# Kernel tuning notes

Hardware: AMD Instinct MI355X
Metric: run time of the kernel (lower is better)

## Reference

```python
import jax, jax.numpy as jnp
import numpy as np

N = 100000
E = 1600000
EPS = 1e-5

def setup_inputs() -> dict:
    key = jax.random.key(0)
    ks = jax.random.split(key, 10)
    d_in, d_h, d_out = 128, 128, 64
    sc = lambda d: 1.0 / np.sqrt(d)
    return {
        "x": jax.random.normal(ks[0], (N, d_in), jnp.float32),
        "edge_src": jax.random.randint(ks[1], (E,), 0, N, jnp.int32),
        "edge_dst": jax.random.randint(ks[2], (E,), 0, N, jnp.int32),
        "Wr0": jax.random.normal(ks[3], (d_in, d_h), jnp.float32) * sc(d_in),
        "Wn0": jax.random.normal(ks[4], (d_in, d_h), jnp.float32) * sc(d_in),
        "b0": jnp.zeros((d_h,), jnp.float32),
        "g0": jnp.ones((d_h,), jnp.float32),
        "be0": jnp.zeros((d_h,), jnp.float32),
        "Wr1": jax.random.normal(ks[5], (d_h, d_h), jnp.float32) * sc(d_h),
        "Wn1": jax.random.normal(ks[6], (d_h, d_h), jnp.float32) * sc(d_h),
        "b1": jnp.zeros((d_h,), jnp.float32),
        "g1": jnp.ones((d_h,), jnp.float32),
        "be1": jnp.zeros((d_h,), jnp.float32),
        "Wr2": jax.random.normal(ks[7], (d_h, d_out), jnp.float32) * sc(d_h),
        "Wn2": jax.random.normal(ks[8], (d_h, d_out), jnp.float32) * sc(d_h),
        "b2": jnp.zeros((d_out,), jnp.float32),
    }

def _mean_agg(x, src, dst):
    # GraphSAGE mean aggregation: scatter-mean of source features onto dst nodes
    deg = jax.ops.segment_sum(jnp.ones((src.shape[0],), x.dtype), dst, num_segments=N)
    s = jax.ops.segment_sum(x[src], dst, num_segments=N)  # [N, d] gather+scatter
    return s / jnp.maximum(deg, 1.0)[:, None]

def _sage_conv(x, src, dst, Wr, Wn, b):
    return x @ Wr + _mean_agg(x, src, dst) @ Wn + b

def _layernorm(h, g, b):
    mu = h.mean(-1, keepdims=True)
    var = ((h - mu) ** 2).mean(-1, keepdims=True)
    return (h - mu) * jax.lax.rsqrt(var + EPS) * g + b

def reference(x, edge_src, edge_dst, Wr0, Wn0, b0, g0, be0,
              Wr1, Wn1, b1, g1, be1, Wr2, Wn2, b2):
    # layer 0: conv -> dropout(eval=identity) -> LayerNorm -> relu
    h = _sage_conv(x, edge_src, edge_dst, Wr0, Wn0, b0)
    h = jax.nn.relu(_layernorm(h, g0, be0))
    # layer 1
    h = _sage_conv(h, edge_src, edge_dst, Wr1, Wn1, b1)
    h = jax.nn.relu(_layernorm(h, g1, be1))
    # final conv + log_softmax over classes
    h = _sage_conv(h, edge_src, edge_dst, Wr2, Wn2, b2)
    return jax.nn.log_softmax(h, axis=1)
```

## Files before the change

### kernel.cpp

```cpp
#include <hip/hip_runtime.h>
#include <math.h>

#define N_NODES 100000
#define NPAD 100032
#define N_EDGES 1600000
#define EPS 1e-5f
#define NC 256
#define CHUNK 6250
#define NR 98
#define RSZ 1024
#define NRC (NR * NC)
#define EIXL_CAP 1792

typedef __bf16 bf16x8 __attribute__((ext_vector_type(8)));
typedef float f32x4 __attribute__((ext_vector_type(4)));
typedef float f32x2 __attribute__((ext_vector_type(2)));

__device__ inline unsigned short f2bf(float f) {
    unsigned u = __float_as_uint(f);
    unsigned r = u + 0x7fffu + ((u >> 16) & 1u);
    return (unsigned short)(r >> 16);
}
__device__ inline float bflo(unsigned u) { return __uint_as_float(u << 16); }
__device__ inline float bfhi(unsigned u) { return __uint_as_float(u & 0xffff0000u); }
__device__ inline unsigned pack2(float lo, float hi) {
    return (unsigned)f2bf(lo) | ((unsigned)f2bf(hi) << 16);
}
__device__ inline unsigned char f2fp8(float f) {
    return (unsigned char)(__builtin_amdgcn_cvt_pk_fp8_f32(f, f, 0, false) & 0xff);
}

__global__ __launch_bounds__(256) void k_prep(const float* __restrict__ x,
                                              unsigned short* __restrict__ xb,
                                              unsigned* __restrict__ xq8,
                                              const int* __restrict__ dst,
                                              int* __restrict__ cntG) {
    __shared__ int hist[NR];
    int t = threadIdx.x;
    if (blockIdx.x < 12500) {
        int idx = blockIdx.x * 256 + t;
        float4 v = ((const float4*)x)[idx];
        ushort4 o;
        o.x = f2bf(v.x); o.y = f2bf(v.y); o.z = f2bf(v.z); o.w = f2bf(v.w);
        ((ushort4*)xb)[idx] = o;
        int q = __builtin_amdgcn_cvt_pk_fp8_f32(v.x, v.y, 0, false);
        q = __builtin_amdgcn_cvt_pk_fp8_f32(v.z, v.w, q, true);
        xq8[idx] = (unsigned)q;
    } else {
        int c = blockIdx.x - 12500;
        for (int i = t; i < NR; i += 256) hist[i] = 0;
        __syncthreads();
        int base = c * CHUNK;
        for (int i = base + t; i < base + CHUNK; i += 256)
            atomicAdd(&hist[dst[i] >> 10], 1);
        __syncthreads();
        for (int i = t; i < NR; i += 256) cntG[i * NC + c] = hist[i];
    }
}

__global__ __launch_bounds__(256) void k_scanA_prepw(
        int* __restrict__ cntG,
        const float* __restrict__ Wr0, const float* __restrict__ Wn0,
        const float* __restrict__ Wr1, const float* __restrict__ Wn1,
        const float* __restrict__ Wr2, const float* __restrict__ Wn2,
        unsigned short* __restrict__ WT0, unsigned short* __restrict__ WT1,
        unsigned short* __restrict__ WT2) {
    int t = threadIdx.x;
    if (blockIdx.x == 0) {
        __shared__ int ts[256];
        const int PER = NRC / 256;
        int s = 0;
        for (int i = 0; i < PER; ++i) s += cntG[t * PER + i];
        ts[t] = s;
        __syncthreads();
        #pragma unroll
        for (int off = 1; off < 256; off <<= 1) {
            int y = 0;
            if (t >= off) y = ts[t - off];
            __syncthreads();
            if (t >= off) ts[t] += y;
            __syncthreads();
        }
        int run = ts[t] - s;
        for (int i = 0; i < PER; ++i) {
            int v = cntG[t * PER + i];
            cntG[t * PER + i] = run;
            run += v;
        }
    } else {
        int b = blockIdx.x - 1;
        if (b < 256) {
            const float* Wr = (b < 128) ? Wr0 : Wr1;
            const float* Wn = (b < 128) ? Wn0 : Wn1;
            unsigned short* WT = (b < 128) ? WT0 : WT1;
            int idx = (b & 127) * 256 + t;
            int n = idx >> 8;
            int kc = idx & 255;
            float v = (kc < 128) ? Wr[kc * 128 + n] : Wn[(kc - 128) * 128 + n];
            WT[idx] = f2bf(v);
        } else {
            int idx = (b - 256) * 256 + t;
            int n = idx >> 7;
            int k = idx & 127;
            float v = (n < 64) ? Wr2[k * 64 + n] : Wn2[k * 64 + (n - 64)];
            WT2[n * 128 + k] = f2bf(v);
        }
    }
}

__global__ __launch_bounds__(1024) void k_bin(const int* __restrict__ src,
                                              const int* __restrict__ dst,
                                              const int* __restrict__ baseG,
                                              unsigned* __restrict__ bpack) {
    __shared__ int cur[NR];
    int t = threadIdx.x, c = blockIdx.x;
    for (int i = t; i < NR; i += 1024) cur[i] = baseG[i * NC + c];
    __syncthreads();
    int base = c * CHUNK;
    for (int i = base + t; i < base + CHUNK; i += 1024) {
        int d = dst[i];
        unsigned s = (unsigned)src[i];
        int p = atomicAdd(&cur[d >> 10], 1);
        bpack[p] = (s << 10) | (unsigned)(d & 1023);
    }
}

__global__ __launch_bounds__(1024) void k_nodeplace(
        const unsigned* __restrict__ bpack, const int* __restrict__ baseG,
        int* __restrict__ deg, float* __restrict__ invdeg,
        int* __restrict__ rowptr, int* __restrict__ eidx) {
    __shared__ int hist[RSZ];
    __shared__ int cur[RSZ];
    __shared__ int wbase[16];
    int r = blockIdx.x, t = threadIdx.x;
    hist[t] = 0;
    __syncthreads();
    int s0 = baseG[r * NC];
    int s1 = (r == NR - 1) ? N_EDGES : baseG[(r + 1) * NC];
    int nbase = r << 10;
    for (int i = s0 + t; i < s1; i += 1024)
        atomicAdd(&hist[bpack[i] & 1023u], 1);
    __syncthreads();
    int lane = t & 63, wv = t >> 6;
    int d = hist[t];
    int s = d;
    #pragma unroll
    for (int m = 1; m < 64; m <<= 1) {
        int y = __shfl_up(s, m);
        if (lane >= m) s += y;
    }
    if (lane == 63) wbase[wv] = s;
    __syncthreads();
    if (t < 16) {
        int v = wbase[t];
        int sv = v;
        #pragma unroll
        for (int m = 1; m < 16; m <<= 1) {
            int y = __shfl_up(sv, m);
            if (t >= m) sv += y;
        }
        wbase[t] = sv - v;
    }
    __syncthreads();
    int p = s0 + wbase[wv] + s - d;
    cur[t] = p;
    int n = nbase + t;
    if (n < N_NODES) {
        rowptr[n] = p;
        deg[n] = d;
        invdeg[n] = 1.0f / fmaxf((float)d, 1.0f);
    }
    __syncthreads();
    for (int i = s0 + t; i < s1; i += 1024) {
        unsigned bp = bpack[i];
        int pp = atomicAdd(&cur[bp & 1023u], 1);
        eidx[pp] = (int)(bp >> 10);
    }
}

__global__ __launch_bounds__(512, 8) void k_gemm_ln(
        const unsigned short* __restrict__ hb,
        const uint4* __restrict__ hq4,
        const int* __restrict__ eidx, const int* __restrict__ rowptr,
        const int* __restrict__ deg, const float* __restrict__ invdeg,
        const unsigned short* __restrict__ WT,
        const float* __restrict__ b, const float* __restrict__ g,
        const float* __restrict__ be, unsigned short* __restrict__ outb,
        unsigned char* __restrict__ outq8) {
    __shared__ unsigned short al[64][136];
    __shared__ unsigned short bt[128][40];
    __shared__ float p1[2][64], p2[2][64];
    __shared__ int eixl[EIXL_CAP];

    const int tid = threadIdx.x;
    const int lane = tid & 63;
    const int w = tid >> 6;
    const int quad = lane >> 4;
    const int l15 = lane & 15;
    const int rt = w >> 1;
    const int ch = w & 1;
    const int row0 = blockIdx.x * 64;

    bf16x8 selfA[4];
    {
        const unsigned short* base = hb + (size_t)(row0 + rt * 16 + l15) * 128 + quad * 8;
        #pragma unroll
        for (int kt = 0; kt < 4; ++kt)
            selfA[kt] = *(const bf16x8*)(base + kt * 32);
    }

    int e0 = rowptr[row0];
    int e1 = (row0 + 64 < N_NODES) ? rowptr[row0 + 64] : N_EDGES;
    int nE = e1 - e0;
    int staged = nE < EIXL_CAP ? nE : EIXL_CAP;
    for (int i = tid; i < staged; i += 512) eixl[i] = eidx[e0 + i];
    __syncthreads();

    {
        int r = tid >> 3;
        int l = tid & 7;
        int node = row0 + r;
        uint4 o0 = {0, 0, 0, 0}, o1 = {0, 0, 0, 0};
        if (node < N_NODES) {
            int start = rowptr[node];
            int cnt = deg[node];
            int rel = start - e0;
            f32x2 a[8];
            #pragma unroll
            for (int i = 0; i < 8; ++i) a[i] = (f32x2)0.0f;
            auto accum = [&](uint4 u) {
                a[0] += __builtin_amdgcn_cvt_pk_f32_fp8((int)u.x, false);
                a[1] += __builtin_amdgcn_cvt_pk_f32_fp8((int)u.x, true);
                a[2] += __builtin_amdgcn_cvt_pk_f32_fp8((int)u.y, false);
                a[3] += __builtin_amdgcn_cvt_pk_f32_fp8((int)u.y, true);
                a[4] += __builtin_amdgcn_cvt_pk_f32_fp8((int)u.z, false);
                a[5] += __builtin_amdgcn_cvt_pk_f32_fp8((int)u.z, true);
                a[6] += __builtin_amdgcn_cvt_pk_f32_fp8((int)u.w, false);
                a[7] += __builtin_amdgcn_cvt_pk_f32_fp8((int)u.w, true);
            };
            if (rel + cnt <= staged) {
                int j = 0;
                for (; j + 4 <= cnt; j += 4) {
                    int i0 = eixl[rel + j + 0], i1 = eixl[rel + j + 1];
                    int i2 = eixl[rel + j + 2], i3 = eixl[rel + j + 3];
                    uint4 u0 = hq4[(unsigned)(i0 * 8 + l)];
                    uint4 u1 = hq4[(unsigned)(i1 * 8 + l)];
                    uint4 u2 = hq4[(unsigned)(i2 * 8 + l)];
                    uint4 u3 = hq4[(unsigned)(i3 * 8 + l)];
                    accum(u0); accum(u1); accum(u2); accum(u3);
                }
                for (; j < cnt; ++j) {
                    uint4 u = hq4[(unsigned)(eixl[rel + j] * 8 + l)];
                    accum(u);
                }
            } else {
                int j = 0;
                for (; j + 4 <= cnt; j += 4) {
                    int s0 = eidx[start + j];
                    int s1 = eidx[start + j + 1];
                    int s2 = eidx[start + j + 2];
                    int s3 = eidx[start + j + 3];
                    uint4 u0 = hq4[(unsigned)(s0 * 8 + l)];
                    uint4 u1 = hq4[(unsigned)(s1 * 8 + l)];
                    uint4 u2 = hq4[(unsigned)(s2 * 8 + l)];
                    uint4 u3 = hq4[(unsigned)(s3 * 8 + l)];
                    accum(u0); accum(u1); accum(u2); accum(u3);
                }
                for (; j < cnt; ++j) {
                    uint4 u = hq4[(unsigned)(eidx[start + j] * 8 + l)];
                    accum(u);
                }
            }
            float id = invdeg[node];
            o0.x = pack2(a[0].x * id, a[0].y * id);
            o0.y = pack2(a[1].x * id, a[1].y * id);
            o0.z = pack2(a[2].x * id, a[2].y * id);
            o0.w = pack2(a[3].x * id, a[3].y * id);
            o1.x = pack2(a[4].x * id, a[4].y * id);
            o1.y = pack2(a[5].x * id, a[5].y * id);
            o1.z = pack2(a[6].x * id, a[6].y * id);
            o1.w = pack2(a[7].x * id, a[7].y * id);
        }
        *(uint4*)&al[r][l * 16] = o0;
        *(uint4*)&al[r][l * 16 + 8] = o1;
    }

    f32x4 acc[4];
    #pragma unroll
    for (int t = 0; t < 4; ++t)
        #pragma unroll
        for (int r = 0; r < 4; ++r) acc[t][r] = 0.0f;

    #pragma unroll
    for (int kt = 0; kt < 8; ++kt) {
        __syncthreads();
        {
            int n = tid >> 2;
            int c = tid & 3;
            *(float4*)&bt[n][c * 8] = ((const float4*)WT)[n * 32 + kt * 4 + c];
        }
        __syncthreads();
        bf16x8 a = (kt < 4)
            ? selfA[kt]
            : *(const bf16x8*)&al[rt * 16 + l15][(kt - 4) * 32 + quad * 8];
        #pragma unroll
        for (int t = 0; t < 4; ++t) {
            bf16x8 bb = *(const bf16x8*)&bt[ch * 64 + t * 16 + l15][quad * 8];
            acc[t] = __builtin_amdgcn_mfma_f32_16x16x32_bf16(a, bb, acc[t], 0, 0, 0);
        }
    }

    float bcol[4], gc[4], bec[4];
    #pragma unroll
    for (int t = 0; t < 4; ++t) {
        int col = ch * 64 + t * 16 + l15;
        bcol[t] = b[col]; gc[t] = g[col]; bec[t] = be[col];
    }
    float v[4][4];
    float s1[4], s2[4];
    #pragma unroll
    for (int r = 0; r < 4; ++r) { s1[r] = 0.0f; s2[r] = 0.0f; }
    #pragma unroll
    for (int t = 0; t < 4; ++t)
        #pragma unroll
        for (int r = 0; r < 4; ++r) {
            float x = acc[t][r] + bcol[t];
            v[t][r] = x;
            s1[r] += x;
            s2[r] += x * x;
        }
    #pragma unroll
    for (int m = 1; m <= 8; m <<= 1)
        #pragma unroll
        for (int r = 0; r < 4; ++r) {
            s1[r] += __shfl_xor(s1[r], m);
            s2[r] += __shfl_xor(s2[r], m);
        }
    if (l15 == 0) {
        #pragma unroll
        for (int r = 0; r < 4; ++r) {
            int rl = rt * 16 + quad * 4 + r;
            p1[ch][rl] = s1[r];
            p2[ch][rl] = s2[r];
        }
    }
    __syncthreads();
    #pragma unroll
    for (int r = 0; r < 4; ++r) {
        int rl = rt * 16 + quad * 4 + r;
        float S1 = p1[0][rl] + p1[1][rl];
        float S2 = p2[0][rl] + p2[1][rl];
        float mean = S1 * (1.0f / 128.0f);
        float var = S2 * (1.0f / 128.0f) - mean * mean;
        float rstd = rsqrtf(var + EPS);
        #pragma unroll
        for (int t = 0; t < 4; ++t) {
            int col = ch * 64 + t * 16 + l15;
            float o = fmaxf((v[t][r] - mean) * rstd * gc[t] + bec[t], 0.0f);
            outb[(size_t)(row0 + rl) * 128 + col] = f2bf(o);
            if (outq8) outq8[(size_t)(row0 + rl) * 128 + col] = f2fp8(o);
        }
    }
}

__global__ __launch_bounds__(512) void k_gemm2(
        const unsigned short* __restrict__ hb, const unsigned short* __restrict__ WT,
        const float* __restrict__ b2, unsigned short* __restrict__ zb16,
        unsigned char* __restrict__ yq8) {
    __shared__ unsigned short hl[64][136];
    __shared__ unsigned short bt[128][136];

    const int tid = threadIdx.x;
    const int lane = tid & 63;
    const int w = tid >> 6;
    const int quad = lane >> 4;
    const int l15 = lane & 15;
    const int rt = w >> 1;
    const int ch = w & 1;
    const int row0 = blockIdx.x * 64;

    #pragma unroll
    for (int t = 0; t < 2; ++t) {
        int idx = tid + t * 512;
        int r = idx >> 4;
        int c8 = idx & 15;
        *(float4*)&hl[r][c8 * 8] = ((const float4*)hb)[(size_t)(row0 + r) * 16 + c8];
    }
    #pragma unroll
    for (int t = 0; t < 4; ++t) {
        int idx = tid + t * 512;
        int n = idx >> 4;
        int c8 = idx & 15;
        *(float4*)&bt[n][c8 * 8] = ((const float4*)WT)[n * 16 + c8];
    }
    __syncthreads();

    f32x4 acc[4];
    #pragma unroll
    for (int t = 0; t < 4; ++t)
        #pragma unroll
        for (int r = 0; r < 4; ++r) acc[t][r] = 0.0f;

    #pragma unroll
    for (int ks = 0; ks < 4; ++ks) {
        bf16x8 a = *(const bf16x8*)&hl[rt * 16 + l15][ks * 32 + quad * 8];
        #pragma unroll
        for (int t = 0; t < 4; ++t) {
            bf16x8 bb = *(const bf16x8*)&bt[ch * 64 + t * 16 + l15][ks * 32 + quad * 8];
            acc[t] = __builtin_amdgcn_mfma_f32_16x16x32_bf16(a, bb, acc[t], 0, 0, 0);
        }
    }

    if (ch == 0) {
        #pragma unroll
        for (int t = 0; t < 4; ++t) {
            int col = t * 16 + l15;
            float bc = b2[col];
            #pragma unroll
            for (int r = 0; r < 4; ++r) {
                int rl = rt * 16 + quad * 4 + r;
                zb16[(size_t)(row0 + rl) * 64 + col] = f2bf(acc[t][r] + bc);
            }
        }
    } else {
        #pragma unroll
        for (int t = 0; t < 4; ++t) {
            int col = t * 16 + l15;
            #pragma unroll
            for (int r = 0; r < 4; ++r) {
                int rl = rt * 16 + quad * 4 + r;
                yq8[(size_t)(row0 + rl) * 64 + col] = f2fp8(acc[t][r]);
            }
        }
    }
}

__global__ __launch_bounds__(256) void k_l2g(const uint4* __restrict__ yq4,
                                             const unsigned short* __restrict__ zb16,
                                             const int* __restrict__ eidx,
                                             const int* __restrict__ rowptr,
                                             const int* __restrict__ deg,
                                             const float* __restrict__ invdeg,
                                             float* __restrict__ out) {
    __shared__ int eixl[EIXL_CAP];
    int node0 = blockIdx.x * 64;
    int e0 = rowptr[node0];
    int e1 = (node0 + 64 < N_NODES) ? rowptr[node0 + 64] : N_EDGES;
    int nE = e1 - e0;
    int staged = nE < EIXL_CAP ? nE : EIXL_CAP;
    for (int i = threadIdx.x; i < staged; i += 256) eixl[i] = eidx[e0 + i];
    __syncthreads();

    int node = node0 + (threadIdx.x >> 2);
    if (node >= N_NODES) return;
    int l = threadIdx.x & 3;
    int start = rowptr[node];
    int cnt = deg[node];
    int rel = start - e0;
    f32x2 a[8];
    #pragma unroll
    for (int i = 0; i < 8; ++i) a[i] = (f32x2)0.0f;

    auto accum = [&](uint4 u) {
        a[0] += __builtin_amdgcn_cvt_pk_f32_fp8((int)u.x, false);
        a[1] += __builtin_amdgcn_cvt_pk_f32_fp8((int)u.x, true);
        a[2] += __builtin_amdgcn_cvt_pk_f32_fp8((int)u.y, false);
        a[3] += __builtin_amdgcn_cvt_pk_f32_fp8((int)u.y, true);
        a[4] += __builtin_amdgcn_cvt_pk_f32_fp8((int)u.z, false);
        a[5] += __builtin_amdgcn_cvt_pk_f32_fp8((int)u.z, true);
        a[6] += __builtin_amdgcn_cvt_pk_f32_fp8((int)u.w, false);
        a[7] += __builtin_amdgcn_cvt_pk_f32_fp8((int)u.w, true);
    };

    if (rel + cnt <= staged) {
        int nb = cnt >> 3;
        for (int bq = 0; bq < nb; ++bq) {
            int jb = rel + bq * 8;
            int i0 = eixl[jb + 0], i1 = eixl[jb + 1];
            int i2 = eixl[jb + 2], i3 = eixl[jb + 3];
            int i4 = eixl[jb + 4], i5 = eixl[jb + 5];
            int i6 = eixl[jb + 6], i7 = eixl[jb + 7];
            uint4 u0 = yq4[(unsigned)(i0 * 4 + l)];
            uint4 u1 = yq4[(unsigned)(i1 * 4 + l)];
            uint4 u2 = yq4[(unsigned)(i2 * 4 + l)];
            uint4 u3 = yq4[(unsigned)(i3 * 4 + l)];
            uint4 u4 = yq4[(unsigned)(i4 * 4 + l)];
            uint4 u5 = yq4[(unsigned)(i5 * 4 + l)];
            uint4 u6 = yq4[(unsigned)(i6 * 4 + l)];
            uint4 u7 = yq4[(unsigned)(i7 * 4 + l)];
            accum(u0); accum(u1); accum(u2); accum(u3);
            accum(u4); accum(u5); accum(u6); accum(u7);
        }
        int j = nb << 3;
        int rem = cnt - j;
        #pragma unroll
        for (int k = 0; k < 8; ++k) {
            if (k < rem) {
                uint4 u = yq4[(unsigned)(eixl[rel + j + k] * 4 + l)];
                accum(u);
            }
        }
    } else {
        int j = 0;
        for (; j + 4 <= cnt; j += 4) {
            int s0 = eidx[start + j];
            int s1 = eidx[start + j + 1];
            int s2 = eidx[start + j + 2];
            int s3 = eidx[start + j + 3];
            uint4 u0 = yq4[(unsigned)(s0 * 4 + l)];
            uint4 u1 = yq4[(unsigned)(s1 * 4 + l)];
            uint4 u2 = yq4[(unsigned)(s2 * 4 + l)];
            uint4 u3 = yq4[(unsigned)(s3 * 4 + l)];
            accum(u0); accum(u1); accum(u2); accum(u3);
        }
        for (; j < cnt; ++j) {
            uint4 u = yq4[(unsigned)(eidx[start + j] * 4 + l)];
            accum(u);
        }
    }

    float id = invdeg[node];
    uint4 z0 = ((const uint4*)zb16)[(size_t)node * 8 + l * 2];
    uint4 z1 = ((const uint4*)zb16)[(size_t)node * 8 + l * 2 + 1];
    float v[16];
    v[0]  = bflo(z0.x) + a[0].x * id; v[1]  = bfhi(z0.x) + a[0].y * id;
    v[2]  = bflo(z0.y) + a[1].x * id; v[3]  = bfhi(z0.y) + a[1].y * id;
    v[4]  = bflo(z0.z) + a[2].x * id; v[5]  = bfhi(z0.z) + a[2].y * id;
    v[6]  = bflo(z0.w) + a[3].x * id; v[7]  = bfhi(z0.w) + a[3].y * id;
    v[8]  = bflo(z1.x) + a[4].x * id; v[9]  = bfhi(z1.x) + a[4].y * id;
    v[10] = bflo(z1.y) + a[5].x * id; v[11] = bfhi(z1.y) + a[5].y * id;
    v[12] = bflo(z1.z) + a[6].x * id; v[13] = bfhi(z1.z) + a[6].y * id;
    v[14] = bflo(z1.w) + a[7].x * id; v[15] = bfhi(z1.w) + a[7].y * id;

    float m = v[0];
    #pragma unroll
    for (int i = 1; i < 16; ++i) m = fmaxf(m, v[i]);
    m = fmaxf(m, __shfl_xor(m, 1));
    m = fmaxf(m, __shfl_xor(m, 2));
    float s = 0.0f;
    #pragma unroll
    for (int i = 0; i < 16; ++i) s += __expf(v[i] - m);
    s += __shfl_xor(s, 1);
    s += __shfl_xor(s, 2);
    float L = m + logf(s);
    #pragma unroll
    for (int k = 0; k < 4; ++k) {
        float4 o;
        o.x = v[4 * k] - L; o.y = v[4 * k + 1] - L;
        o.z = v[4 * k + 2] - L; o.w = v[4 * k + 3] - L;
        ((float4*)out)[(size_t)node * 16 + l * 4 + k] = o;
    }
}

extern "C" void kernel_launch(void* const* d_in, const int* in_sizes, int n_in,
                              void* d_out, int out_size, void* d_ws, size_t ws_size,
                              hipStream_t stream) {
    const float* x   = (const float*)d_in[0];
    const int* esrc  = (const int*)d_in[1];
    const int* edst  = (const int*)d_in[2];
    const float* Wr0 = (const float*)d_in[3];
    const float* Wn0 = (const float*)d_in[4];
    const float* b0  = (const float*)d_in[5];
    const float* g0  = (const float*)d_in[6];
    const float* be0 = (const float*)d_in[7];
    const float* Wr1 = (const float*)d_in[8];
    const float* Wn1 = (const float*)d_in[9];
    const float* b1  = (const float*)d_in[10];
    const float* g1  = (const float*)d_in[11];
    const float* be1 = (const float*)d_in[12];
    const float* Wr2 = (const float*)d_in[13];
    const float* Wn2 = (const float*)d_in[14];
    const float* b2  = (const float*)d_in[15];
    float* out = (float*)d_out;

    char* p = (char*)d_ws;
    auto alloc = [&](size_t bytes) {
        void* r = (void*)p;
        p += (bytes + 255) & ~(size_t)255;
        return r;
    };
    int*   deg    = (int*)  alloc(N_NODES * 4);
    float* invdeg = (float*)alloc(N_NODES * 4);
    int*   rowptr = (int*)  alloc(N_NODES * 4);
    int*   cntG   = (int*)  alloc(NRC * 4);
    unsigned* bpack = (unsigned*)alloc((size_t)N_EDGES * 4);
    int*   eidx   = (int*)  alloc((size_t)N_EDGES * 4);
    unsigned short* xb   = (unsigned short*)alloc((size_t)NPAD * 128 * 2);
    unsigned short* h1   = (unsigned short*)alloc((size_t)NPAD * 128 * 2);
    unsigned*       xq8  = (unsigned*)      alloc((size_t)N_NODES * 128);
    unsigned char*  h1q8 = (unsigned char*) alloc((size_t)NPAD * 128);
    unsigned short* zb16 = (unsigned short*)alloc((size_t)NPAD * 64 * 2);
    unsigned char*  yq8  = (unsigned char*) alloc((size_t)NPAD * 64);
    unsigned short* WT0  = (unsigned short*)alloc(128 * 256 * 2);
    unsigned short* WT1  = (unsigned short*)alloc(128 * 256 * 2);
    unsigned short* WT2  = (unsigned short*)alloc(128 * 128 * 2);

    k_prep<<<12500 + NC, 256, 0, stream>>>(x, xb, xq8, edst, cntG);
    k_scanA_prepw<<<321, 256, 0, stream>>>(cntG, Wr0, Wn0, Wr1, Wn1, Wr2, Wn2,
                                           WT0, WT1, WT2);
    k_bin<<<NC, 1024, 0, stream>>>(esrc, edst, cntG, bpack);
    k_nodeplace<<<NR, 1024, 0, stream>>>(bpack, cntG, deg, invdeg, rowptr, eidx);

    k_gemm_ln<<<NPAD / 64, 512, 0, stream>>>(xb, (const uint4*)xq8, eidx, rowptr,
                                             deg, invdeg, WT0, b0, g0, be0, h1, h1q8);

    k_gemm_ln<<<NPAD / 64, 512, 0, stream>>>(h1, (const uint4*)h1q8, eidx, rowptr,
                                             deg, invdeg, WT1, b1, g1, be1, xb,
                                             (unsigned char*)nullptr);

    k_gemm2<<<NPAD / 64, 512, 0, stream>>>(xb, WT2, b2, zb16, yq8);
    k_l2g<<<(N_NODES + 63) / 64, 256, 0, stream>>>((const uint4*)yq8, zb16, eidx, rowptr, deg, invdeg, out);
}
```

Before: 320.1 us.

## Fuse final layer GEMM into second gemm_ln kernel epilogue

The layer-2 GEMM (projecting the normalized hidden state into the self and neighbor 64-wide outputs) is folded into the second k_gemm_ln call. The LayerNorm+ReLU output is written to shared memory instead of global bf16, then multiplied against WT2 read directly from global memory. This removes one kernel launch and a full write and re-read of the 100k x 128 bf16 hidden tensor. In exchange, launch bounds drop from 8 to 6 waves per SIMD to leave room for extra registers, and B-operand loads now hit global/cache rather than LDS.

```diff
diff --git a/kernel.cpp b/kernel.cpp
--- a/kernel.cpp
+++ b/kernel.cpp
@@ -178,7 +178,7 @@
     }
 }
 
-__global__ __launch_bounds__(512, 8) void k_gemm_ln(
+__global__ __launch_bounds__(512, 6) void k_gemm_ln(
         const unsigned short* __restrict__ hb,
         const uint4* __restrict__ hq4,
         const int* __restrict__ eidx, const int* __restrict__ rowptr,
@@ -186,7 +186,11 @@
         const unsigned short* __restrict__ WT,
         const float* __restrict__ b, const float* __restrict__ g,
         const float* __restrict__ be, unsigned short* __restrict__ outb,
-        unsigned char* __restrict__ outq8) {
+        unsigned char* __restrict__ outq8,
+        const unsigned short* __restrict__ WT2,
+        const float* __restrict__ b2,
+        unsigned short* __restrict__ zb16,
+        unsigned char* __restrict__ yq8) {
     __shared__ unsigned short al[64][136];
     __shared__ unsigned short bt[128][40];
     __shared__ float p1[2][64], p2[2][64];
@@ -357,79 +361,52 @@
         for (int t = 0; t < 4; ++t) {
             int col = ch * 64 + t * 16 + l15;
             float o = fmaxf((v[t][r] - mean) * rstd * gc[t] + bec[t], 0.0f);
-            outb[(size_t)(row0 + rl) * 128 + col] = f2bf(o);
-            if (outq8) outq8[(size_t)(row0 + rl) * 128 + col] = f2fp8(o);
-        }
-    }
-}
-
-__global__ __launch_bounds__(512) void k_gemm2(
-        const unsigned short* __restrict__ hb, const unsigned short* __restrict__ WT,
-        const float* __restrict__ b2, unsigned short* __restrict__ zb16,
-        unsigned char* __restrict__ yq8) {
-    __shared__ unsigned short hl[64][136];
-    __shared__ unsigned short bt[128][136];
-
-    const int tid = threadIdx.x;
-    const int lane = tid & 63;
-    const int w = tid >> 6;
-    const int quad = lane >> 4;
-    const int l15 = lane & 15;
-    const int rt = w >> 1;
-    const int ch = w & 1;
-    const int row0 = blockIdx.x * 64;
-
-    #pragma unroll
-    for (int t = 0; t < 2; ++t) {
-        int idx = tid + t * 512;
-        int r = idx >> 4;
-        int c8 = idx & 15;
-        *(float4*)&hl[r][c8 * 8] = ((const float4*)hb)[(size_t)(row0 + r) * 16 + c8];
-    }
-    #pragma unroll
-    for (int t = 0; t < 4; ++t) {
-        int idx = tid + t * 512;
-        int n = idx >> 4;
-        int c8 = idx & 15;
-        *(float4*)&bt[n][c8 * 8] = ((const float4*)WT)[n * 16 + c8];
-    }
-    __syncthreads();
-
-    f32x4 acc[4];
-    #pragma unroll
-    for (int t = 0; t < 4; ++t)
-        #pragma unroll
-        for (int r = 0; r < 4; ++r) acc[t][r] = 0.0f;
-
-    #pragma unroll
-    for (int ks = 0; ks < 4; ++ks) {
-        bf16x8 a = *(const bf16x8*)&hl[rt * 16 + l15][ks * 32 + quad * 8];
-        #pragma unroll
-        for (int t = 0; t < 4; ++t) {
-            bf16x8 bb = *(const bf16x8*)&bt[ch * 64 + t * 16 + l15][ks * 32 + quad * 8];
-            acc[t] = __builtin_amdgcn_mfma_f32_16x16x32_bf16(a, bb, acc[t], 0, 0, 0);
-        }
-    }
-
-    if (ch == 0) {
-        #pragma unroll
-        for (int t = 0; t < 4; ++t) {
-            int col = t * 16 + l15;
-            float bc = b2[col];
+            if (!WT2) {
+                outb[(size_t)(row0 + rl) * 128 + col] = f2bf(o);
+                if (outq8) outq8[(size_t)(row0 + rl) * 128 + col] = f2fp8(o);
+            } else {
+                al[rl][col] = f2bf(o);
+            }
+        }
+    }
+
+    if (WT2) {
+        __syncthreads();
+        f32x4 acc2[4];
+        #pragma unroll
+        for (int t = 0; t < 4; ++t)
             #pragma unroll
-            for (int r = 0; r < 4; ++r) {
-                int rl = rt * 16 + quad * 4 + r;
-                zb16[(size_t)(row0 + rl) * 64 + col] = f2bf(acc[t][r] + bc);
+            for (int r = 0; r < 4; ++r) acc2[t][r] = 0.0f;
+        #pragma unroll
+        for (int kt = 0; kt < 4; ++kt) {
+            bf16x8 a = *(const bf16x8*)&al[rt * 16 + l15][kt * 32 + quad * 8];
+            #pragma unroll
+            for (int t = 0; t < 4; ++t) {
+                bf16x8 bb = *(const bf16x8*)(WT2 +
+                    (size_t)(ch * 64 + t * 16 + l15) * 128 + kt * 32 + quad * 8);
+                acc2[t] = __builtin_amdgcn_mfma_f32_16x16x32_bf16(a, bb, acc2[t], 0, 0, 0);
             }
         }
-    } else {
-        #pragma unroll
-        for (int t = 0; t < 4; ++t) {
-            int col = t * 16 + l15;
+        if (ch == 0) {
             #pragma unroll
-            for (int r = 0; r < 4; ++r) {
-                int rl = rt * 16 + quad * 4 + r;
-                yq8[(size_t)(row0 + rl) * 64 + col] = f2fp8(acc[t][r]);
+            for (int t = 0; t < 4; ++t) {
+                int col = t * 16 + l15;
+                float bc = b2[col];
+                #pragma unroll
+                for (int r = 0; r < 4; ++r) {
+                    int rl = rt * 16 + quad * 4 + r;
+                    zb16[(size_t)(row0 + rl) * 64 + col] = f2bf(acc2[t][r] + bc);
+                }
+            }
+        } else {
+            #pragma unroll
+            for (int t = 0; t < 4; ++t) {
+                int col = t * 16 + l15;
+                #pragma unroll
+                for (int r = 0; r < 4; ++r) {
+                    int rl = rt * 16 + quad * 4 + r;
+                    yq8[(size_t)(row0 + rl) * 64 + col] = f2fp8(acc2[t][r]);
+                }
             }
         }
     }
@@ -602,12 +579,17 @@
     k_nodeplace<<<NR, 1024, 0, stream>>>(bpack, cntG, deg, invdeg, rowptr, eidx);
 
     k_gemm_ln<<<NPAD / 64, 512, 0, stream>>>(xb, (const uint4*)xq8, eidx, rowptr,
-                                             deg, invdeg, WT0, b0, g0, be0, h1, h1q8);
+                                             deg, invdeg, WT0, b0, g0, be0, h1, h1q8,
+                                             (const unsigned short*)nullptr,
+                                             (const float*)nullptr,
+                                             (unsigned short*)nullptr,
+                                             (unsigned char*)nullptr);
 
     k_gemm_ln<<<NPAD / 64, 512, 0, stream>>>(h1, (const uint4*)h1q8, eidx, rowptr,
-                                             deg, invdeg, WT1, b1, g1, be1, xb,
-                                             (unsigned char*)nullptr);
-
-    k_gemm2<<<NPAD / 64, 512, 0, stream>>>(xb, WT2, b2, zb16, yq8);
+                                             deg, invdeg, WT1, b1, g1, be1,
+                                             (unsigned short*)nullptr,
+                                             (unsigned char*)nullptr,
+                                             WT2, b2, zb16, yq8);
+
     k_l2g<<<(N_NODES + 63) / 64, 256, 0, stream>>>((const uint4*)yq8, zb16, eidx, rowptr, deg, invdeg, out);
 }
```

Result: slower. 340.8 us (+6.5%).
